# Kernel optimization log

Hardware: AMD Instinct MI355X
Metric: run time of the kernel (lower is better)

The kernel has to match this reference:

```python
import jax, jax.numpy as jnp
import numpy as np

IN_FEATURES = 4096
OUT_FEATURES = 11008
B, S = 8, 512


def setup_inputs() -> dict:
    key = jax.random.key(0)
    k1, k2, k3 = jax.random.split(key, 3)
    x = jax.random.normal(k1, (B, S, IN_FEATURES), dtype=jnp.float32)
    # int8 weights simulated as int32 values in [-127, 127]
    weight_int8 = jax.random.randint(k2, (OUT_FEATURES, IN_FEATURES), -127, 128, dtype=jnp.int32)
    # per-output-channel scales (positive, small, like absmax/127)
    weight_scale = jax.random.uniform(k3, (OUT_FEATURES,), dtype=jnp.float32) * 0.01 + 1e-4
    return {"x": x, "weight_int8": weight_int8, "weight_scale": weight_scale}


def reference(x, weight_int8, weight_scale):
    # On-the-fly dequantization: W[o, i] = int8[o, i] * scale[o]
    weight = weight_int8.astype(x.dtype) * weight_scale.astype(x.dtype)[:, None]
    # F.linear: y = x @ W^T  -> [B, S, out_features]
    return jnp.einsum('bsi,oi->bso', x, weight)
```

## Files before the change

### kernel.cpp

```cpp
#include <hip/hip_runtime.h>
#include <stdint.h>

#define M_DIM 4096
#define N_DIM 11008
#define K_DIM 4096

typedef int i32x4 __attribute__((ext_vector_type(4)));

static __device__ __forceinline__ void direct_load16(const void* gptr, void* ldsptr) {
    __builtin_amdgcn_global_load_lds(
        (const __attribute__((address_space(1))) void*)gptr,
        (__attribute__((address_space(3))) void*)ldsptr,
        16, 0, 0);
}

__global__ __launch_bounds__(256) void cvt_w_kernel(const int* __restrict__ w,
                                                    int8_t* __restrict__ o) {
    int t = blockIdx.x * 256 + threadIdx.x;
    const int4* w4 = (const int4*)w;
    int4 a = w4[t];
    ((unsigned*)o)[t] = (a.x & 255) | ((a.y & 255) << 8) | ((a.z & 255) << 16) | (a.w << 24);
}

__global__ __launch_bounds__(256) void quant_x_kernel(const float* __restrict__ x,
                                                      int8_t* __restrict__ xq,
                                                      float* __restrict__ xs) {
    __shared__ float wmax[4];
    const int row = blockIdx.x;
    const int t = threadIdx.x;
    const float4* xr = (const float4*)(x + (size_t)row * K_DIM);

    float4 v[4];
    float am = 0.0f;
#pragma unroll
    for (int p = 0; p < 4; p++) {
        v[p] = xr[p * 256 + t];
        am = fmaxf(am, fmaxf(fmaxf(fabsf(v[p].x), fabsf(v[p].y)),
                             fmaxf(fabsf(v[p].z), fabsf(v[p].w))));
    }
#pragma unroll
    for (int o = 32; o > 0; o >>= 1)
        am = fmaxf(am, __shfl_xor(am, o));
    if ((t & 63) == 0) wmax[t >> 6] = am;
    __syncthreads();
    am = fmaxf(fmaxf(wmax[0], wmax[1]), fmaxf(wmax[2], wmax[3]));

    const float inv = 127.0f / am;
    int* oq = (int*)(xq + (size_t)row * K_DIM);
#pragma unroll
    for (int p = 0; p < 4; p++) {
        int qa = (int)rintf(v[p].x * inv);
        int qb = (int)rintf(v[p].y * inv);
        int qc = (int)rintf(v[p].z * inv);
        int qd = (int)rintf(v[p].w * inv);
        oq[p * 256 + t] = (qa & 255) | ((qb & 255) << 8) | ((qc & 255) << 16) | (qd << 24);
    }
    if (t == 0) xs[row] = am * (1.0f / 127.0f);
}


__global__ __launch_bounds__(512, 2) void gemm_i8_kernel(
    const int8_t* __restrict__ A,
    const int8_t* __restrict__ B,
    const float* __restrict__ xs,
    const float* __restrict__ ws,
    float* __restrict__ C)
{
    __shared__ __align__(16) int8_t As[4][256 * 64];
    __shared__ __align__(16) int8_t Bs[4][256 * 64];

    const int tid  = threadIdx.x;
    const int lane = tid & 63;
    const int wave = tid >> 6;
    const int wm   = wave >> 2;
    const int wn   = wave & 3;
    const int quad = lane >> 4;
    const int r16  = lane & 15;

    const int orig = blockIdx.x + (blockIdx.y << 4);
    const int work = (orig & 7) * 86 + (orig >> 3);
    const int m0 = (work & 15) * 256;
    const int n0 = (work >> 4) * 256;

    const int srow   = tid >> 2;
    const int schunk = (tid & 3) ^ ((tid >> 3) & 3);
    const int8_t* gA = A + (size_t)(m0 + srow) * K_DIM + schunk * 16;
    const int8_t* gB = B + (size_t)(n0 + srow) * K_DIM + schunk * 16;
    const size_t half2 = (size_t)128 * K_DIM;
    const int wb = wave * 1024;

    const int fsw   = (r16 >> 1) & 3;
    const int a_off = (wm * 128 + r16) * 64 + ((quad ^ fsw) * 16);
    const int b_off = (wn * 64  + r16) * 64 + ((quad ^ fsw) * 16);

    i32x4 acc[8][4];
#pragma unroll
    for (int i = 0; i < 8; i++)
#pragma unroll
        for (int j = 0; j < 4; j++) acc[i][j] = (i32x4)(0);

    i32x4 afX[4], afY[4], bfA[4], bfB[4];

#define STAGE_A(t, buf) do {                                                  \
        direct_load16(gA + (size_t)(t) * 64,         (char*)As[buf] + wb);    \
        direct_load16(gA + (size_t)(t) * 64 + half2, (char*)As[buf] + wb + 8192); \
    } while (0)
#define STAGE_B(t, buf) do {                                                  \
        direct_load16(gB + (size_t)(t) * 64,         (char*)Bs[buf] + wb);    \
        direct_load16(gB + (size_t)(t) * 64 + half2, (char*)Bs[buf] + wb + 8192); \
    } while (0)

#define LDA4(dst, buf, fb) do {                                               \
        const int8_t* _p = As[buf];                                           \
        _Pragma("unroll")                                                     \
        for (int _i = 0; _i < 4; _i++)                                        \
            dst[_i] = *(const i32x4*)(_p + a_off + ((fb) + _i) * 1024);       \
    } while (0)
#define LDB2(dst, buf, j0) do {                                               \
        const int8_t* _p = Bs[buf];                                           \
        dst[(j0)]     = *(const i32x4*)(_p + b_off + ((j0)) * 1024);          \
        dst[(j0) + 1] = *(const i32x4*)(_p + b_off + ((j0) + 1) * 1024);      \
    } while (0)
#define MM(AF, BF, H) do {                                                    \
        __builtin_amdgcn_s_setprio(1);                                        \
        _Pragma("unroll")                                                     \
        for (int _i = 0; _i < 4; _i++)                                        \
            _Pragma("unroll")                                                 \
            for (int _j = 0; _j < 4; _j++)                                    \
                acc[(H) * 4 + _i][_j] = __builtin_amdgcn_mfma_i32_16x16x64_i8(\
                    AF[_i], BF[_j], acc[(H) * 4 + _i][_j], 0, 0, 0);          \
        __builtin_amdgcn_s_setprio(0);                                        \
        asm volatile("s_waitcnt vmcnt(4)" ::: "memory");                      \
        __builtin_amdgcn_s_barrier();                                         \
    } while (0)

    STAGE_A(0, 0); STAGE_B(0, 0);
    STAGE_A(1, 1); STAGE_B(1, 1);
    STAGE_A(2, 2); STAGE_B(2, 2);
    asm volatile("s_waitcnt vmcnt(4)" ::: "memory");
    __builtin_amdgcn_s_barrier();

    LDA4(afX, 0, 0);
    LDB2(bfA, 0, 0); LDB2(bfA, 0, 2);

    for (int u = 0; u < 32; ++u) {
        const int t0 = 2 * u, t1 = t0 + 1;
        const int b0 = t0 & 3, b1 = t1 & 3, b2 = (t0 + 2) & 3;
        const int sb0 = (t0 + 3) & 3, sb1 = (t0 + 4) & 3;
        const int s0 = (t0 + 3 > 63) ? 63 : t0 + 3;
        const int s1 = (t0 + 4 > 63) ? 63 : t0 + 4;

        LDA4(afY, b0, 4); LDB2(bfB, b1, 0); STAGE_A(s0, sb0); MM(afX, bfA, 0);
        LDA4(afX, b1, 0); LDB2(bfB, b1, 2); STAGE_B(s0, sb0); MM(afY, bfA, 1);
        LDA4(afY, b1, 4); LDB2(bfA, b2, 0); STAGE_A(s1, sb1); MM(afX, bfB, 0);
        LDA4(afX, b2, 0); LDB2(bfA, b2, 2); STAGE_B(s1, sb1); MM(afY, bfB, 1);
    }

#undef MM
#undef LDB2
#undef LDA4
#undef STAGE_B
#undef STAGE_A

#pragma unroll
    for (int i = 0; i < 8; i++) {
        const int mrow = m0 + wm * 128 + i * 16 + quad * 4;
        float rsc[4];
#pragma unroll
        for (int r = 0; r < 4; r++) rsc[r] = xs[mrow + r];
#pragma unroll
        for (int j = 0; j < 4; j++) {
            const int n = n0 + wn * 64 + j * 16 + r16;
            const float s = ws[n];
#pragma unroll
            for (int r = 0; r < 4; r++)
                C[(size_t)(mrow + r) * N_DIM + n] = (float)acc[i][j][r] * s * rsc[r];
        }
    }
}


extern "C" void kernel_launch(void* const* d_in, const int* in_sizes, int n_in,
                              void* d_out, int out_size, void* d_ws, size_t ws_size,
                              hipStream_t stream) {
    const float* x       = (const float*)d_in[0];
    const int*   w_int   = (const int*)d_in[1];
    const float* w_scale = (const float*)d_in[2];
    float*       out     = (float*)d_out;

    int8_t* wq = (int8_t*)d_ws;
    int8_t* xq = (int8_t*)((char*)d_ws + (size_t)N_DIM * K_DIM);
    float*  xs = (float*)((char*)d_ws + (size_t)N_DIM * K_DIM + (size_t)M_DIM * K_DIM);

    cvt_w_kernel<<<dim3(N_DIM * K_DIM / 4 / 256), dim3(256), 0, stream>>>(w_int, wq);
    quant_x_kernel<<<dim3(M_DIM), dim3(256), 0, stream>>>(x, xq, xs);
    gemm_i8_kernel<<<dim3(M_DIM / 256, N_DIM / 256), dim3(512), 0, stream>>>(xq, wq, xs, w_scale, out);
}
```

Before: 542.0 us.

## Switch GEMM inner loop from 16x16x64 to 32x32x32 int8 MFMA

Replaces the 16x16x64 int8 matrix instructions with 32x32x32 ones, reorganizing the per-wave accumulators into 4x2 tiles of 32x32. The LDS fragment loads, the swizzle chunk selection and the epilogue mapping are rewritten to match the new operand and output layouts. Larger MFMA tiles need fewer LDS fragment reads per multiply and fewer instructions per K step. The 32x32 form has longer instruction latency, and the new swizzle must still avoid bank conflicts.

```diff
diff --git a/kernel.cpp b/kernel.cpp
--- a/kernel.cpp
+++ b/kernel.cpp
@@ -5,7 +5,8 @@
 #define N_DIM 11008
 #define K_DIM 4096
 
-typedef int i32x4 __attribute__((ext_vector_type(4)));
+typedef int i32x4  __attribute__((ext_vector_type(4)));
+typedef int i32x16 __attribute__((ext_vector_type(16)));
 
 static __device__ __forceinline__ void direct_load16(const void* gptr, void* ldsptr) {
     __builtin_amdgcn_global_load_lds(
@@ -74,8 +75,8 @@
     const int wave = tid >> 6;
     const int wm   = wave >> 2;
     const int wn   = wave & 3;
-    const int quad = lane >> 4;
-    const int r16  = lane & 15;
+    const int r32  = lane & 31;
+    const int g    = lane >> 5;
 
     const int orig = blockIdx.x + (blockIdx.y << 4);
     const int work = (orig & 7) * 86 + (orig >> 3);
@@ -89,17 +90,19 @@
     const size_t half2 = (size_t)128 * K_DIM;
     const int wb = wave * 1024;
 
-    const int fsw   = (r16 >> 1) & 3;
-    const int a_off = (wm * 128 + r16) * 64 + ((quad ^ fsw) * 16);
-    const int b_off = (wn * 64  + r16) * 64 + ((quad ^ fsw) * 16);
-
-    i32x4 acc[8][4];
-#pragma unroll
-    for (int i = 0; i < 8; i++)
-#pragma unroll
-        for (int j = 0; j < 4; j++) acc[i][j] = (i32x4)(0);
-
-    i32x4 afX[4], afY[4], bfA[4], bfB[4];
+    const int fsw = (r32 >> 1) & 3;
+    const int ck0 = ((0 + g) ^ fsw) * 16;
+    const int ck1 = ((2 + g) ^ fsw) * 16;
+    const int a_row0 = (wm * 128 + r32) * 64;
+    const int b_row0 = (wn * 64  + r32) * 64;
+
+    i32x16 acc[4][2];
+#pragma unroll
+    for (int i = 0; i < 4; i++)
+#pragma unroll
+        for (int j = 0; j < 2; j++) acc[i][j] = (i32x16)(0);
+
+    i32x4 afX[4], afY[4], bfX[2], bfY[2];
 
 #define STAGE_A(t, buf) do {                                                  \
         direct_load16(gA + (size_t)(t) * 64,         (char*)As[buf] + wb);    \
@@ -110,25 +113,25 @@
         direct_load16(gB + (size_t)(t) * 64 + half2, (char*)Bs[buf] + wb + 8192); \
     } while (0)
 
-#define LDA4(dst, buf, fb) do {                                               \
+#define LDA4(dst, buf, CK) do {                                               \
         const int8_t* _p = As[buf];                                           \
         _Pragma("unroll")                                                     \
         for (int _i = 0; _i < 4; _i++)                                        \
-            dst[_i] = *(const i32x4*)(_p + a_off + ((fb) + _i) * 1024);       \
-    } while (0)
-#define LDB2(dst, buf, j0) do {                                               \
+            dst[_i] = *(const i32x4*)(_p + a_row0 + _i * 2048 + (CK));        \
+    } while (0)
+#define LDB2(dst, buf, CK) do {                                               \
         const int8_t* _p = Bs[buf];                                           \
-        dst[(j0)]     = *(const i32x4*)(_p + b_off + ((j0)) * 1024);          \
-        dst[(j0) + 1] = *(const i32x4*)(_p + b_off + ((j0) + 1) * 1024);      \
-    } while (0)
-#define MM(AF, BF, H) do {                                                    \
+        dst[0] = *(const i32x4*)(_p + b_row0 + (CK));                         \
+        dst[1] = *(const i32x4*)(_p + b_row0 + 2048 + (CK));                  \
+    } while (0)
+#define MM(AF, BF) do {                                                       \
         __builtin_amdgcn_s_setprio(1);                                        \
         _Pragma("unroll")                                                     \
         for (int _i = 0; _i < 4; _i++)                                        \
             _Pragma("unroll")                                                 \
-            for (int _j = 0; _j < 4; _j++)                                    \
-                acc[(H) * 4 + _i][_j] = __builtin_amdgcn_mfma_i32_16x16x64_i8(\
-                    AF[_i], BF[_j], acc[(H) * 4 + _i][_j], 0, 0, 0);          \
+            for (int _j = 0; _j < 2; _j++)                                    \
+                acc[_i][_j] = __builtin_amdgcn_mfma_i32_32x32x32_i8(          \
+                    AF[_i], BF[_j], acc[_i][_j], 0, 0, 0);                    \
         __builtin_amdgcn_s_setprio(0);                                        \
         asm volatile("s_waitcnt vmcnt(4)" ::: "memory");                      \
         __builtin_amdgcn_s_barrier();                                         \
@@ -140,8 +143,8 @@
     asm volatile("s_waitcnt vmcnt(4)" ::: "memory");
     __builtin_amdgcn_s_barrier();
 
-    LDA4(afX, 0, 0);
-    LDB2(bfA, 0, 0); LDB2(bfA, 0, 2);
+    LDA4(afX, 0, ck0);
+    LDB2(bfX, 0, ck0);
 
     for (int u = 0; u < 32; ++u) {
         const int t0 = 2 * u, t1 = t0 + 1;
@@ -150,10 +153,10 @@
         const int s0 = (t0 + 3 > 63) ? 63 : t0 + 3;
         const int s1 = (t0 + 4 > 63) ? 63 : t0 + 4;
 
-        LDA4(afY, b0, 4); LDB2(bfB, b1, 0); STAGE_A(s0, sb0); MM(afX, bfA, 0);
-        LDA4(afX, b1, 0); LDB2(bfB, b1, 2); STAGE_B(s0, sb0); MM(afY, bfA, 1);
-        LDA4(afY, b1, 4); LDB2(bfA, b2, 0); STAGE_A(s1, sb1); MM(afX, bfB, 0);
-        LDA4(afX, b2, 0); LDB2(bfA, b2, 2); STAGE_B(s1, sb1); MM(afY, bfB, 1);
+        LDA4(afY, b0, ck1); LDB2(bfY, b0, ck1); STAGE_A(s0, sb0); MM(afX, bfX);
+        LDA4(afX, b1, ck0); LDB2(bfX, b1, ck0); STAGE_B(s0, sb0); MM(afY, bfY);
+        LDA4(afY, b1, ck1); LDB2(bfY, b1, ck1); STAGE_A(s1, sb1); MM(afX, bfX);
+        LDA4(afX, b2, ck0); LDB2(bfX, b2, ck0); STAGE_B(s1, sb1); MM(afY, bfY);
     }
 
 #undef MM
@@ -162,19 +165,24 @@
 #undef STAGE_B
 #undef STAGE_A
 
-#pragma unroll
-    for (int i = 0; i < 8; i++) {
-        const int mrow = m0 + wm * 128 + i * 16 + quad * 4;
-        float rsc[4];
-#pragma unroll
-        for (int r = 0; r < 4; r++) rsc[r] = xs[mrow + r];
-#pragma unroll
-        for (int j = 0; j < 4; j++) {
-            const int n = n0 + wn * 64 + j * 16 + r16;
-            const float s = ws[n];
-#pragma unroll
-            for (int r = 0; r < 4; r++)
-                C[(size_t)(mrow + r) * N_DIM + n] = (float)acc[i][j][r] * s * rsc[r];
+    const int g4 = g * 4;
+#pragma unroll
+    for (int ai = 0; ai < 4; ai++) {
+        const int mb = m0 + wm * 128 + ai * 32 + g4;
+#pragma unroll
+        for (int rq = 0; rq < 4; rq++) {
+            float rs[4];
+#pragma unroll
+            for (int rr = 0; rr < 4; rr++) rs[rr] = xs[mb + rq * 8 + rr];
+#pragma unroll
+            for (int bj = 0; bj < 2; bj++) {
+                const int n = n0 + wn * 64 + bj * 32 + r32;
+                const float s = ws[n];
+#pragma unroll
+                for (int rr = 0; rr < 4; rr++)
+                    C[(size_t)(mb + rq * 8 + rr) * N_DIM + n] =
+                        (float)acc[ai][bj][rq * 4 + rr] * s * rs[rr];
+            }
         }
     }
 }
```

Measured after the change: 562.0 us. 3.7% more time.
